# Optimization experiments

Measured on AMD Instinct MI355X. Metric: run time of the kernel, lower is better.

Reference implementation:

```python
import jax, jax.numpy as jnp
import numpy as np

D_MODEL = 1024
N_HEADS = 16
D_HEAD = 64


def setup_inputs() -> dict:
    key = jax.random.key(0)
    kx, kq, kk, kv, ko = jax.random.split(key, 5)
    B, T = 2, 2048
    inner = N_HEADS * D_HEAD
    s = 1.0 / np.sqrt(D_MODEL)
    return {
        "x": jax.random.normal(kx, (B, T, D_MODEL), dtype=jnp.float32),
        "Wq": jax.random.normal(kq, (D_MODEL, inner), dtype=jnp.float32) * s,
        "Wk": jax.random.normal(kk, (D_MODEL, inner), dtype=jnp.float32) * s,
        "Wv": jax.random.normal(kv, (D_MODEL, inner), dtype=jnp.float32) * s,
        "Wo": jax.random.normal(ko, (inner, D_MODEL), dtype=jnp.float32) * (1.0 / np.sqrt(inner)),
    }


def reference(x, Wq, Wk, Wv, Wo):
    B, T, D = x.shape
    H, d = N_HEADS, D_HEAD
    q = (x @ Wq).reshape(B, T, H, d)
    k = (x @ Wk).reshape(B, T, H, d)
    v = (x @ Wv).reshape(B, T, H, d)
    # scale=False -> no 1/sqrt(d) scaling
    scores = jnp.einsum('bthd,bshd->bhts', q, k)
    # strictly-lower-triangular mask (tril with diagonal=-1): s < t kept
    mask = jnp.tril(jnp.ones((T, T), dtype=bool), k=-1)
    scores = jnp.where(mask, scores, 0.0)
    out = jnp.einsum('bhts,bshd->bthd', scores, v).reshape(B, T, H * d)
    return out @ Wo
```

## Files before the change

kernel.cpp:

```cpp
#include <hip/hip_runtime.h>
#include <hip/hip_bf16.h>

#define TSEQ   2048
#define DM     1024
#define NHEAD  16
#define DH     64
#define BATCH  2
#define MR     (BATCH * TSEQ)
#define CH     64
#define NC     (TSEQ / CH)
#define QKVLD  (3 * DM)
#define LP     72

typedef __attribute__((ext_vector_type(8))) short bf16x8;
typedef __attribute__((ext_vector_type(4))) float f32x4;

__device__ __forceinline__ short f2bf(float x) {
  __hip_bfloat16 h = __float2bfloat16(x);
  return *reinterpret_cast<short*>(&h);
}

__device__ __forceinline__ void stage16(const void* g, void* l) {
  __builtin_amdgcn_global_load_lds(
      (const __attribute__((address_space(1))) void*)g,
      (__attribute__((address_space(3))) void*)l, 16, 0, 0);
}

__device__ __forceinline__ void store_elem(float v, float* p) { *p = v; }
__device__ __forceinline__ void store_elem(float v, __hip_bfloat16* p) { *p = __float2bfloat16(v); }

template <typename OutT>
__global__ __launch_bounds__(256) void gemm_bf16(const short* __restrict__ A,
                                                 const short* __restrict__ Bt,
                                                 OutT* __restrict__ C,
                                                 int M, int N, int K, int ldc) {
  __shared__ short As[128][32];
  __shared__ short Bs[128][32];
  const int tid = threadIdx.x;
  const int lane = tid & 63, wid = tid >> 6;
  const int wave_m = wid >> 1, wave_n = wid & 1;
  const int row0 = blockIdx.y * 128, col0 = blockIdx.x * 128;

  const int sr = tid >> 2, sk = (tid & 3) * 8;
  const short* Ag0 = A + (size_t)(row0 + sr) * K + sk;
  const short* Bg0 = Bt + (size_t)(col0 + sr) * K + sk;
  short* AsL = &As[0][0] + tid * 8;
  short* BsL = &Bs[0][0] + tid * 8;

  f32x4 acc[4][4];
#pragma unroll
  for (int i = 0; i < 4; ++i)
#pragma unroll
    for (int j = 0; j < 4; ++j) acc[i][j] = (f32x4){0.f, 0.f, 0.f, 0.f};

  const int fm = wave_m * 64 + (lane & 15);
  const int fn = wave_n * 64 + (lane & 15);
  const int fk = (lane >> 4) * 8;

  for (int k0 = 0; k0 < K; k0 += 32) {
    stage16(Ag0 + k0, AsL);
    stage16(Ag0 + (size_t)64 * K + k0, AsL + 2048);
    stage16(Bg0 + k0, BsL);
    stage16(Bg0 + (size_t)64 * K + k0, BsL + 2048);
    __syncthreads();
    bf16x8 af[4], bf[4];
#pragma unroll
    for (int t = 0; t < 4; ++t) {
      af[t] = *(const bf16x8*)&As[fm + t * 16][fk];
      bf[t] = *(const bf16x8*)&Bs[fn + t * 16][fk];
    }
#pragma unroll
    for (int im = 0; im < 4; ++im)
#pragma unroll
      for (int jn = 0; jn < 4; ++jn)
        acc[im][jn] = __builtin_amdgcn_mfma_f32_16x16x32_bf16(af[im], bf[jn], acc[im][jn], 0, 0, 0);
    __syncthreads();
  }

  const int crow = (lane >> 4) * 4, ccol = lane & 15;
#pragma unroll
  for (int im = 0; im < 4; ++im)
#pragma unroll
    for (int jn = 0; jn < 4; ++jn) {
      OutT* Cp = C + (size_t)(row0 + wave_m * 64 + im * 16 + crow) * ldc
                   + col0 + wave_n * 64 + jn * 16 + ccol;
#pragma unroll
      for (int r = 0; r < 4; ++r) store_elem(acc[im][jn][r], Cp + (size_t)r * ldc);
    }
}

__global__ __launch_bounds__(256) void cvt_bf16(const float* __restrict__ in,
                                                __hip_bfloat16* __restrict__ out, int n) {
  int i = (blockIdx.x * 256 + threadIdx.x) * 4;
  if (i >= n) return;
  float4 v = *(const float4*)(in + i);
  union { __hip_bfloat16 h[4]; uint2 u; } pk;
  pk.h[0] = __float2bfloat16(v.x); pk.h[1] = __float2bfloat16(v.y);
  pk.h[2] = __float2bfloat16(v.z); pk.h[3] = __float2bfloat16(v.w);
  *(uint2*)(out + i) = pk.u;
}

__global__ __launch_bounds__(256) void transposeW4(const float* __restrict__ W0,
                                                   const float* __restrict__ W1,
                                                   const float* __restrict__ W2,
                                                   const float* __restrict__ W3,
                                                   __hip_bfloat16* __restrict__ Wt) {
  const float* W = blockIdx.z == 0 ? W0 : blockIdx.z == 1 ? W1 : blockIdx.z == 2 ? W2 : W3;
  __hip_bfloat16* out = Wt + (size_t)blockIdx.z * DM * DM;
  __shared__ float tile[64][65];
  const int tid = threadIdx.x;
  const int kt = blockIdx.y * 64, nt = blockIdx.x * 64;
  const int lr = tid >> 6, lc = tid & 63;
#pragma unroll
  for (int i = 0; i < 16; ++i) {
    int k = i * 4 + lr;
    tile[k][lc] = W[(size_t)(kt + k) * DM + nt + lc];
  }
  __syncthreads();
  const int nl = tid >> 4, k4 = (tid & 15) * 4;
#pragma unroll
  for (int i = 0; i < 4; ++i) {
    int n = i * 16 + nl;
    union { __hip_bfloat16 h[4]; uint2 u; } pk;
#pragma unroll
    for (int x = 0; x < 4; ++x) pk.h[x] = __float2bfloat16(tile[k4 + x][n]);
    *(uint2*)(out + (size_t)(nt + n) * DM + kt + k4) = pk.u;
  }
}

__global__ __launch_bounds__(256) void chunk_kv(const __hip_bfloat16* __restrict__ QKV,
                                                float* __restrict__ Mc) {
  const int c = blockIdx.x, h = blockIdx.y, b = blockIdx.z;
  __shared__ short Kt[DH][LP];
  __shared__ short Vt[DH][LP];
  const int tid = threadIdx.x;
  const int lane = tid & 63, w = tid >> 6;
  const int r = tid >> 2, q16 = (tid & 3) * 16;
  const short* qkv = (const short*)QKV;
  const size_t grow = ((size_t)(b * TSEQ + c * CH + r)) * QKVLD + h * DH;
  short kk[16], vv[16];
  *(bf16x8*)&kk[0] = *(const bf16x8*)(qkv + grow + DM + q16);
  *(bf16x8*)&kk[8] = *(const bf16x8*)(qkv + grow + DM + q16 + 8);
  *(bf16x8*)&vv[0] = *(const bf16x8*)(qkv + grow + 2 * DM + q16);
  *(bf16x8*)&vv[8] = *(const bf16x8*)(qkv + grow + 2 * DM + q16 + 8);
#pragma unroll
  for (int j = 0; j < 16; ++j) {
    Kt[q16 + j][r] = kk[j];
    Vt[q16 + j][r] = vv[j];
  }
  __syncthreads();

  const int m = lane & 15, q = lane >> 4;
  bf16x8 af[2];
  af[0] = *(const bf16x8*)&Vt[16 * w + m][q * 8];
  af[1] = *(const bf16x8*)&Vt[16 * w + m][q * 8 + 32];
  f32x4 acc[4];
#pragma unroll
  for (int ct = 0; ct < 4; ++ct) acc[ct] = (f32x4){0.f, 0.f, 0.f, 0.f};
#pragma unroll
  for (int ct = 0; ct < 4; ++ct) {
    bf16x8 b0 = *(const bf16x8*)&Kt[ct * 16 + m][q * 8];
    bf16x8 b1 = *(const bf16x8*)&Kt[ct * 16 + m][q * 8 + 32];
    acc[ct] = __builtin_amdgcn_mfma_f32_16x16x32_bf16(af[0], b0, acc[ct], 0, 0, 0);
    acc[ct] = __builtin_amdgcn_mfma_f32_16x16x32_bf16(af[1], b1, acc[ct], 0, 0, 0);
  }
  float* out = Mc + ((size_t)((b * NHEAD + h) * NC + c)) * (DH * DH);
#pragma unroll
  for (int ct = 0; ct < 4; ++ct)
#pragma unroll
    for (int rr = 0; rr < 4; ++rr) {
      int row = 16 * w + q * 4 + rr, col = ct * 16 + m;
      out[(size_t)row * DH + col] = acc[ct][rr];
    }
}

__global__ __launch_bounds__(256) void scan_states(const float* __restrict__ Mc,
                                                   __hip_bfloat16* __restrict__ Spre) {
  const int bh = blockIdx.y;
  const size_t off = (size_t)bh * NC * (DH * DH) + blockIdx.x * 256 + threadIdx.x;
  const float* src = Mc + off;
  __hip_bfloat16* dst = Spre + off;
  float run = 0.f;
  for (int c = 0; c < NC; ++c) {
    dst[(size_t)c * (DH * DH)] = __float2bfloat16(run);
    run += src[(size_t)c * (DH * DH)];
  }
}

__global__ __launch_bounds__(256) void intra_attn(const __hip_bfloat16* __restrict__ QKV,
                                                  const __hip_bfloat16* __restrict__ Spre,
                                                  __hip_bfloat16* __restrict__ O_) {
  const int c = blockIdx.x, h = blockIdx.y, b = blockIdx.z;
  __shared__ short Qs[CH][LP];
  __shared__ short Ks[CH][LP];
  __shared__ short Vt[DH][LP];
  __shared__ short St[DH][LP];
  const int tid = threadIdx.x;
  const int lane = tid & 63, w = tid >> 6;
  const int r = tid >> 2, q16 = (tid & 3) * 16;
  const short* qkv = (const short*)QKV;
  const size_t grow = ((size_t)(b * TSEQ + c * CH + r)) * QKVLD + h * DH;
  *(bf16x8*)&Qs[r][q16]     = *(const bf16x8*)(qkv + grow + q16);
  *(bf16x8*)&Qs[r][q16 + 8] = *(const bf16x8*)(qkv + grow + q16 + 8);
  *(bf16x8*)&Ks[r][q16]     = *(const bf16x8*)(qkv + grow + DM + q16);
  *(bf16x8*)&Ks[r][q16 + 8] = *(const bf16x8*)(qkv + grow + DM + q16 + 8);
  const short* Sg = (const short*)Spre + ((size_t)((b * NHEAD + h) * NC + c)) * (DH * DH);
  *(bf16x8*)&St[r][q16]     = *(const bf16x8*)(Sg + r * DH + q16);
  *(bf16x8*)&St[r][q16 + 8] = *(const bf16x8*)(Sg + r * DH + q16 + 8);
  short vv[16];
  *(bf16x8*)&vv[0] = *(const bf16x8*)(qkv + grow + 2 * DM + q16);
  *(bf16x8*)&vv[8] = *(const bf16x8*)(qkv + grow + 2 * DM + q16 + 8);
#pragma unroll
  for (int j = 0; j < 16; ++j) Vt[q16 + j][r] = vv[j];
  __syncthreads();

  const int m = lane & 15, q = lane >> 4;
  bf16x8 af[2];
  af[0] = *(const bf16x8*)&Qs[16 * w + m][q * 8];
  af[1] = *(const bf16x8*)&Qs[16 * w + m][q * 8 + 32];
  f32x4 acc[4], pacc[4];
#pragma unroll
  for (int ct = 0; ct < 4; ++ct) {
    acc[ct] = (f32x4){0.f, 0.f, 0.f, 0.f};
    pacc[ct] = (f32x4){0.f, 0.f, 0.f, 0.f};
  }
#pragma unroll
  for (int ct = 0; ct < 4; ++ct) {
    bf16x8 s0 = *(const bf16x8*)&St[ct * 16 + m][q * 8];
    bf16x8 s1 = *(const bf16x8*)&St[ct * 16 + m][q * 8 + 32];
    acc[ct] = __builtin_amdgcn_mfma_f32_16x16x32_bf16(af[0], s0, acc[ct], 0, 0, 0);
    acc[ct] = __builtin_amdgcn_mfma_f32_16x16x32_bf16(af[1], s1, acc[ct], 0, 0, 0);
    bf16x8 k0 = *(const bf16x8*)&Ks[ct * 16 + m][q * 8];
    bf16x8 k1 = *(const bf16x8*)&Ks[ct * 16 + m][q * 8 + 32];
    pacc[ct] = __builtin_amdgcn_mfma_f32_16x16x32_bf16(af[0], k0, pacc[ct], 0, 0, 0);
    pacc[ct] = __builtin_amdgcn_mfma_f32_16x16x32_bf16(af[1], k1, pacc[ct], 0, 0, 0);
  }
  __syncthreads();
#pragma unroll
  for (int ct = 0; ct < 4; ++ct) {
    int col = ct * 16 + m;
#pragma unroll
    for (int rr = 0; rr < 4; ++rr) {
      int row = 16 * w + q * 4 + rr;
      float pv = (col < row) ? pacc[ct][rr] : 0.f;
      Qs[row][col] = f2bf(pv);
    }
  }
  __syncthreads();
  bf16x8 pf[2];
  pf[0] = *(const bf16x8*)&Qs[16 * w + m][q * 8];
  pf[1] = *(const bf16x8*)&Qs[16 * w + m][q * 8 + 32];
#pragma unroll
  for (int ct = 0; ct < 4; ++ct) {
    bf16x8 v0 = *(const bf16x8*)&Vt[ct * 16 + m][q * 8];
    bf16x8 v1 = *(const bf16x8*)&Vt[ct * 16 + m][q * 8 + 32];
    acc[ct] = __builtin_amdgcn_mfma_f32_16x16x32_bf16(pf[0], v0, acc[ct], 0, 0, 0);
    acc[ct] = __builtin_amdgcn_mfma_f32_16x16x32_bf16(pf[1], v1, acc[ct], 0, 0, 0);
  }
  __hip_bfloat16* Ob = O_ + ((size_t)(b * TSEQ + c * CH)) * DM + h * DH;
#pragma unroll
  for (int ct = 0; ct < 4; ++ct)
#pragma unroll
    for (int rr = 0; rr < 4; ++rr) {
      int row = 16 * w + q * 4 + rr, col = ct * 16 + m;
      Ob[(size_t)row * DM + col] = __float2bfloat16(acc[ct][rr]);
    }
}

extern "C" void kernel_launch(void* const* d_in, const int* in_sizes, int n_in,
                              void* d_out, int out_size, void* d_ws, size_t ws_size,
                              hipStream_t stream) {
  const float* x  = (const float*)d_in[0];
  const float* Wq = (const float*)d_in[1];
  const float* Wk = (const float*)d_in[2];
  const float* Wv = (const float*)d_in[3];
  const float* Wo = (const float*)d_in[4];
  float* out = (float*)d_out;

  char* ws = (char*)d_ws;
  __hip_bfloat16* xb    = (__hip_bfloat16*)ws;  ws += (size_t)MR * DM * 2;
  __hip_bfloat16* WtAll = (__hip_bfloat16*)ws;  ws += (size_t)4 * DM * DM * 2;
  __hip_bfloat16* qkvb  = (__hip_bfloat16*)ws;  ws += (size_t)MR * QKVLD * 2;
  float*          Mc    = (float*)ws;           ws += (size_t)BATCH * NHEAD * NC * DH * DH * 4;
  __hip_bfloat16* Spre  = (__hip_bfloat16*)ws;  ws += (size_t)BATCH * NHEAD * NC * DH * DH * 2;
  __hip_bfloat16* aob   = (__hip_bfloat16*)ws;  ws += (size_t)MR * DM * 2;

  cvt_bf16<<<(MR * DM / 4 + 255) / 256, 256, 0, stream>>>(x, xb, MR * DM);
  transposeW4<<<dim3(DM / 64, DM / 64, 4), 256, 0, stream>>>(Wq, Wk, Wv, Wo, WtAll);

  gemm_bf16<__hip_bfloat16><<<dim3(QKVLD / 128, MR / 128), 256, 0, stream>>>(
      (const short*)xb, (const short*)WtAll, qkvb, MR, QKVLD, DM, QKVLD);

  chunk_kv<<<dim3(NC, NHEAD, BATCH), 256, 0, stream>>>(qkvb, Mc);
  scan_states<<<dim3(DH * DH / 256, BATCH * NHEAD), 256, 0, stream>>>(Mc, Spre);
  intra_attn<<<dim3(NC, NHEAD, BATCH), 256, 0, stream>>>(qkvb, Spre, aob);

  gemm_bf16<float><<<dim3(DM / 128, MR / 128), 256, 0, stream>>>(
      (const short*)aob, (const short*)(WtAll + (size_t)3 * DM * DM), out, MR, DM, DM, DM);
}
```

Baseline: 170.2 us.

## Emit chunk-transposed K/V from QKV GEMM and merge prep kernels

The QKV GEMM epilogue now writes Q and K row-major and also writes K and V in per-(batch, head, chunk) transposed 64x64 tiles. chunk_kv and intra_attn can then read MFMA fragments straight from global memory, with no LDS transposes and fewer barriers. intra_attn is reordered to compute transposed outputs so it can use packed stores. The x conversion and weight transposes are merged into one prep launch. The cost is extra global writes of K, plus more workspace and 8-byte strided scattered stores in the GEMM epilogue.

```diff
diff --git a/kernel.cpp b/kernel.cpp
--- a/kernel.cpp
+++ b/kernel.cpp
@@ -26,14 +26,13 @@
       (__attribute__((address_space(3))) void*)l, 16, 0, 0);
 }
 
-__device__ __forceinline__ void store_elem(float v, float* p) { *p = v; }
-__device__ __forceinline__ void store_elem(float v, __hip_bfloat16* p) { *p = __float2bfloat16(v); }
-
-template <typename OutT>
-__global__ __launch_bounds__(256) void gemm_bf16(const short* __restrict__ A,
-                                                 const short* __restrict__ Bt,
-                                                 OutT* __restrict__ C,
-                                                 int M, int N, int K, int ldc) {
+__global__ __launch_bounds__(256) void gemm_qkv(const short* __restrict__ A,
+                                                const short* __restrict__ Bt,
+                                                short* __restrict__ qb,
+                                                short* __restrict__ kb,
+                                                short* __restrict__ kT,
+                                                short* __restrict__ vT) {
+  const int K = DM;
   __shared__ short As[128][32];
   __shared__ short Bs[128][32];
   const int tid = threadIdx.x;
@@ -78,37 +77,127 @@
   }
 
   const int crow = (lane >> 4) * 4, ccol = lane & 15;
+  const int region = col0 >> 10;
+
+  if (region <= 1) {
+    short* Cb = (region == 0) ? qb : kb;
+#pragma unroll
+    for (int im = 0; im < 4; ++im)
+#pragma unroll
+      for (int jn = 0; jn < 4; ++jn) {
+        const int gr = row0 + wave_m * 64 + im * 16 + crow;
+        const int gc = (col0 & 1023) + wave_n * 64 + jn * 16 + ccol;
+        short* Cp = Cb + (size_t)gr * DM + gc;
+#pragma unroll
+        for (int r = 0; r < 4; ++r) Cp[(size_t)r * DM] = f2bf(acc[im][jn][r]);
+      }
+  }
+  if (region >= 1) {
+    short* Tt = (region == 1) ? kT : vT;
+    const int gr0 = row0 + wave_m * 64;
+    const int b = gr0 >> 11;
+    const int c = (gr0 & 2047) >> 6;
+#pragma unroll
+    for (int im = 0; im < 4; ++im)
+#pragma unroll
+      for (int jn = 0; jn < 4; ++jn) {
+        const int gcol = (col0 & 1023) + wave_n * 64 + jn * 16 + ccol;
+        const int h = gcol >> 6, i = gcol & 63;
+        const int s0 = im * 16 + crow;
+        size_t idx = ((((size_t)(b * NHEAD + h) * NC + c) * DH + i) * DH + s0);
+        union { short h4[4]; uint2 u; } pk;
+#pragma unroll
+        for (int r = 0; r < 4; ++r) pk.h4[r] = f2bf(acc[im][jn][r]);
+        *(uint2*)(Tt + idx) = pk.u;
+      }
+  }
+}
+
+__global__ __launch_bounds__(256) void gemm_out(const short* __restrict__ A,
+                                                const short* __restrict__ Bt,
+                                                float* __restrict__ C) {
+  const int K = DM, N = DM;
+  __shared__ short As[128][32];
+  __shared__ short Bs[128][32];
+  const int tid = threadIdx.x;
+  const int lane = tid & 63, wid = tid >> 6;
+  const int wave_m = wid >> 1, wave_n = wid & 1;
+  const int row0 = blockIdx.y * 128, col0 = blockIdx.x * 128;
+
+  const int sr = tid >> 2, sk = (tid & 3) * 8;
+  const short* Ag0 = A + (size_t)(row0 + sr) * K + sk;
+  const short* Bg0 = Bt + (size_t)(col0 + sr) * K + sk;
+  short* AsL = &As[0][0] + tid * 8;
+  short* BsL = &Bs[0][0] + tid * 8;
+
+  f32x4 acc[4][4];
+#pragma unroll
+  for (int i = 0; i < 4; ++i)
+#pragma unroll
+    for (int j = 0; j < 4; ++j) acc[i][j] = (f32x4){0.f, 0.f, 0.f, 0.f};
+
+  const int fm = wave_m * 64 + (lane & 15);
+  const int fn = wave_n * 64 + (lane & 15);
+  const int fk = (lane >> 4) * 8;
+
+  for (int k0 = 0; k0 < K; k0 += 32) {
+    stage16(Ag0 + k0, AsL);
+    stage16(Ag0 + (size_t)64 * K + k0, AsL + 2048);
+    stage16(Bg0 + k0, BsL);
+    stage16(Bg0 + (size_t)64 * K + k0, BsL + 2048);
+    __syncthreads();
+    bf16x8 af[4], bf[4];
+#pragma unroll
+    for (int t = 0; t < 4; ++t) {
+      af[t] = *(const bf16x8*)&As[fm + t * 16][fk];
+      bf[t] = *(const bf16x8*)&Bs[fn + t * 16][fk];
+    }
+#pragma unroll
+    for (int im = 0; im < 4; ++im)
+#pragma unroll
+      for (int jn = 0; jn < 4; ++jn)
+        acc[im][jn] = __builtin_amdgcn_mfma_f32_16x16x32_bf16(af[im], bf[jn], acc[im][jn], 0, 0, 0);
+    __syncthreads();
+  }
+
+  const int crow = (lane >> 4) * 4, ccol = lane & 15;
 #pragma unroll
   for (int im = 0; im < 4; ++im)
 #pragma unroll
     for (int jn = 0; jn < 4; ++jn) {
-      OutT* Cp = C + (size_t)(row0 + wave_m * 64 + im * 16 + crow) * ldc
-                   + col0 + wave_n * 64 + jn * 16 + ccol;
-#pragma unroll
-      for (int r = 0; r < 4; ++r) store_elem(acc[im][jn][r], Cp + (size_t)r * ldc);
-    }
-}
-
-__global__ __launch_bounds__(256) void cvt_bf16(const float* __restrict__ in,
-                                                __hip_bfloat16* __restrict__ out, int n) {
-  int i = (blockIdx.x * 256 + threadIdx.x) * 4;
-  if (i >= n) return;
-  float4 v = *(const float4*)(in + i);
-  union { __hip_bfloat16 h[4]; uint2 u; } pk;
-  pk.h[0] = __float2bfloat16(v.x); pk.h[1] = __float2bfloat16(v.y);
-  pk.h[2] = __float2bfloat16(v.z); pk.h[3] = __float2bfloat16(v.w);
-  *(uint2*)(out + i) = pk.u;
-}
-
-__global__ __launch_bounds__(256) void transposeW4(const float* __restrict__ W0,
-                                                   const float* __restrict__ W1,
-                                                   const float* __restrict__ W2,
-                                                   const float* __restrict__ W3,
-                                                   __hip_bfloat16* __restrict__ Wt) {
+      float* Cp = C + (size_t)(row0 + wave_m * 64 + im * 16 + crow) * N
+                    + col0 + wave_n * 64 + jn * 16 + ccol;
+#pragma unroll
+      for (int r = 0; r < 4; ++r) Cp[(size_t)r * N] = acc[im][jn][r];
+    }
+}
+
+__global__ __launch_bounds__(256) void prep(const float* __restrict__ x,
+                                            const float* __restrict__ W0,
+                                            const float* __restrict__ W1,
+                                            const float* __restrict__ W2,
+                                            const float* __restrict__ W3,
+                                            __hip_bfloat16* __restrict__ xb,
+                                            __hip_bfloat16* __restrict__ Wt) {
+  const int tid = threadIdx.x;
+  if (blockIdx.z == 4) {
+    const int bid = blockIdx.y * 16 + blockIdx.x;
+    const float* src = x + (size_t)bid * 16384;
+    __hip_bfloat16* dst = xb + (size_t)bid * 16384;
+#pragma unroll
+    for (int it = 0; it < 16; ++it) {
+      int i = it * 1024 + tid * 4;
+      float4 v = *(const float4*)(src + i);
+      union { __hip_bfloat16 h[4]; uint2 u; } pk;
+      pk.h[0] = __float2bfloat16(v.x); pk.h[1] = __float2bfloat16(v.y);
+      pk.h[2] = __float2bfloat16(v.z); pk.h[3] = __float2bfloat16(v.w);
+      *(uint2*)(dst + i) = pk.u;
+    }
+    return;
+  }
   const float* W = blockIdx.z == 0 ? W0 : blockIdx.z == 1 ? W1 : blockIdx.z == 2 ? W2 : W3;
   __hip_bfloat16* out = Wt + (size_t)blockIdx.z * DM * DM;
   __shared__ float tile[64][65];
-  const int tid = threadIdx.x;
   const int kt = blockIdx.y * 64, nt = blockIdx.x * 64;
   const int lr = tid >> 6, lc = tid & 63;
 #pragma unroll
@@ -123,55 +212,38 @@
     int n = i * 16 + nl;
     union { __hip_bfloat16 h[4]; uint2 u; } pk;
 #pragma unroll
-    for (int x = 0; x < 4; ++x) pk.h[x] = __float2bfloat16(tile[k4 + x][n]);
+    for (int xx = 0; xx < 4; ++xx) pk.h[xx] = __float2bfloat16(tile[k4 + xx][n]);
     *(uint2*)(out + (size_t)(nt + n) * DM + kt + k4) = pk.u;
   }
 }
 
-__global__ __launch_bounds__(256) void chunk_kv(const __hip_bfloat16* __restrict__ QKV,
+__global__ __launch_bounds__(256) void chunk_kv(const short* __restrict__ kT,
+                                                const short* __restrict__ vT,
                                                 float* __restrict__ Mc) {
   const int c = blockIdx.x, h = blockIdx.y, b = blockIdx.z;
-  __shared__ short Kt[DH][LP];
-  __shared__ short Vt[DH][LP];
-  const int tid = threadIdx.x;
-  const int lane = tid & 63, w = tid >> 6;
-  const int r = tid >> 2, q16 = (tid & 3) * 16;
-  const short* qkv = (const short*)QKV;
-  const size_t grow = ((size_t)(b * TSEQ + c * CH + r)) * QKVLD + h * DH;
-  short kk[16], vv[16];
-  *(bf16x8*)&kk[0] = *(const bf16x8*)(qkv + grow + DM + q16);
-  *(bf16x8*)&kk[8] = *(const bf16x8*)(qkv + grow + DM + q16 + 8);
-  *(bf16x8*)&vv[0] = *(const bf16x8*)(qkv + grow + 2 * DM + q16);
-  *(bf16x8*)&vv[8] = *(const bf16x8*)(qkv + grow + 2 * DM + q16 + 8);
-#pragma unroll
-  for (int j = 0; j < 16; ++j) {
-    Kt[q16 + j][r] = kk[j];
-    Vt[q16 + j][r] = vv[j];
-  }
-  __syncthreads();
-
+  const size_t tile = ((size_t)(b * NHEAD + h) * NC + c) * (DH * DH);
+  const int tid = threadIdx.x, lane = tid & 63, w = tid >> 6;
   const int m = lane & 15, q = lane >> 4;
-  bf16x8 af[2];
-  af[0] = *(const bf16x8*)&Vt[16 * w + m][q * 8];
-  af[1] = *(const bf16x8*)&Vt[16 * w + m][q * 8 + 32];
+  const short* vt = vT + tile;
+  const short* kt = kT + tile;
+  bf16x8 a0 = *(const bf16x8*)(vt + (16 * w + m) * DH + q * 8);
+  bf16x8 a1 = *(const bf16x8*)(vt + (16 * w + m) * DH + q * 8 + 32);
   f32x4 acc[4];
 #pragma unroll
   for (int ct = 0; ct < 4; ++ct) acc[ct] = (f32x4){0.f, 0.f, 0.f, 0.f};
 #pragma unroll
   for (int ct = 0; ct < 4; ++ct) {
-    bf16x8 b0 = *(const bf16x8*)&Kt[ct * 16 + m][q * 8];
-    bf16x8 b1 = *(const bf16x8*)&Kt[ct * 16 + m][q * 8 + 32];
-    acc[ct] = __builtin_amdgcn_mfma_f32_16x16x32_bf16(af[0], b0, acc[ct], 0, 0, 0);
-    acc[ct] = __builtin_amdgcn_mfma_f32_16x16x32_bf16(af[1], b1, acc[ct], 0, 0, 0);
-  }
-  float* out = Mc + ((size_t)((b * NHEAD + h) * NC + c)) * (DH * DH);
+    bf16x8 b0 = *(const bf16x8*)(kt + (ct * 16 + m) * DH + q * 8);
+    bf16x8 b1 = *(const bf16x8*)(kt + (ct * 16 + m) * DH + q * 8 + 32);
+    acc[ct] = __builtin_amdgcn_mfma_f32_16x16x32_bf16(a0, b0, acc[ct], 0, 0, 0);
+    acc[ct] = __builtin_amdgcn_mfma_f32_16x16x32_bf16(a1, b1, acc[ct], 0, 0, 0);
+  }
+  float* out = Mc + tile;
 #pragma unroll
   for (int ct = 0; ct < 4; ++ct)
 #pragma unroll
-    for (int rr = 0; rr < 4; ++rr) {
-      int row = 16 * w + q * 4 + rr, col = ct * 16 + m;
-      out[(size_t)row * DH + col] = acc[ct][rr];
-    }
+    for (int rr = 0; rr < 4; ++rr)
+      out[(size_t)(16 * w + q * 4 + rr) * DH + ct * 16 + m] = acc[ct][rr];
 }
 
 __global__ __launch_bounds__(256) void scan_states(const float* __restrict__ Mc,
@@ -187,37 +259,34 @@
   }
 }
 
-__global__ __launch_bounds__(256) void intra_attn(const __hip_bfloat16* __restrict__ QKV,
-                                                  const __hip_bfloat16* __restrict__ Spre,
-                                                  __hip_bfloat16* __restrict__ O_) {
+__global__ __launch_bounds__(256) void intra_attn(const short* __restrict__ qb,
+                                                  const short* __restrict__ kb,
+                                                  const short* __restrict__ vT,
+                                                  const short* __restrict__ Spre,
+                                                  short* __restrict__ O_) {
   const int c = blockIdx.x, h = blockIdx.y, b = blockIdx.z;
   __shared__ short Qs[CH][LP];
   __shared__ short Ks[CH][LP];
-  __shared__ short Vt[DH][LP];
-  __shared__ short St[DH][LP];
-  const int tid = threadIdx.x;
-  const int lane = tid & 63, w = tid >> 6;
+  const int tid = threadIdx.x, lane = tid & 63, w = tid >> 6;
+  const int m = lane & 15, q = lane >> 4;
   const int r = tid >> 2, q16 = (tid & 3) * 16;
-  const short* qkv = (const short*)QKV;
-  const size_t grow = ((size_t)(b * TSEQ + c * CH + r)) * QKVLD + h * DH;
-  *(bf16x8*)&Qs[r][q16]     = *(const bf16x8*)(qkv + grow + q16);
-  *(bf16x8*)&Qs[r][q16 + 8] = *(const bf16x8*)(qkv + grow + q16 + 8);
-  *(bf16x8*)&Ks[r][q16]     = *(const bf16x8*)(qkv + grow + DM + q16);
-  *(bf16x8*)&Ks[r][q16 + 8] = *(const bf16x8*)(qkv + grow + DM + q16 + 8);
-  const short* Sg = (const short*)Spre + ((size_t)((b * NHEAD + h) * NC + c)) * (DH * DH);
-  *(bf16x8*)&St[r][q16]     = *(const bf16x8*)(Sg + r * DH + q16);
-  *(bf16x8*)&St[r][q16 + 8] = *(const bf16x8*)(Sg + r * DH + q16 + 8);
-  short vv[16];
-  *(bf16x8*)&vv[0] = *(const bf16x8*)(qkv + grow + 2 * DM + q16);
-  *(bf16x8*)&vv[8] = *(const bf16x8*)(qkv + grow + 2 * DM + q16 + 8);
-#pragma unroll
-  for (int j = 0; j < 16; ++j) Vt[q16 + j][r] = vv[j];
+  const size_t tile = ((size_t)(b * NHEAD + h) * NC + c) * (DH * DH);
+  const size_t grow = ((size_t)(b * TSEQ + c * CH + r)) * DM + h * DH;
+  *(bf16x8*)&Qs[r][q16]     = *(const bf16x8*)(qb + grow + q16);
+  *(bf16x8*)&Qs[r][q16 + 8] = *(const bf16x8*)(qb + grow + q16 + 8);
+  *(bf16x8*)&Ks[r][q16]     = *(const bf16x8*)(kb + grow + q16);
+  *(bf16x8*)&Ks[r][q16 + 8] = *(const bf16x8*)(kb + grow + q16 + 8);
+  const short* vt = vT + tile;
+  const short* st = Spre + tile;
+  bf16x8 av0 = *(const bf16x8*)(vt + (16 * w + m) * DH + q * 8);
+  bf16x8 av1 = *(const bf16x8*)(vt + (16 * w + m) * DH + q * 8 + 32);
+  bf16x8 as0 = *(const bf16x8*)(st + (16 * w + m) * DH + q * 8);
+  bf16x8 as1 = *(const bf16x8*)(st + (16 * w + m) * DH + q * 8 + 32);
   __syncthreads();
 
-  const int m = lane & 15, q = lane >> 4;
-  bf16x8 af[2];
-  af[0] = *(const bf16x8*)&Qs[16 * w + m][q * 8];
-  af[1] = *(const bf16x8*)&Qs[16 * w + m][q * 8 + 32];
+  bf16x8 aq0 = *(const bf16x8*)&Qs[16 * w + m][q * 8];
+  bf16x8 aq1 = *(const bf16x8*)&Qs[16 * w + m][q * 8 + 32];
+
   f32x4 acc[4], pacc[4];
 #pragma unroll
   for (int ct = 0; ct < 4; ++ct) {
@@ -226,45 +295,41 @@
   }
 #pragma unroll
   for (int ct = 0; ct < 4; ++ct) {
-    bf16x8 s0 = *(const bf16x8*)&St[ct * 16 + m][q * 8];
-    bf16x8 s1 = *(const bf16x8*)&St[ct * 16 + m][q * 8 + 32];
-    acc[ct] = __builtin_amdgcn_mfma_f32_16x16x32_bf16(af[0], s0, acc[ct], 0, 0, 0);
-    acc[ct] = __builtin_amdgcn_mfma_f32_16x16x32_bf16(af[1], s1, acc[ct], 0, 0, 0);
-    bf16x8 k0 = *(const bf16x8*)&Ks[ct * 16 + m][q * 8];
-    bf16x8 k1 = *(const bf16x8*)&Ks[ct * 16 + m][q * 8 + 32];
-    pacc[ct] = __builtin_amdgcn_mfma_f32_16x16x32_bf16(af[0], k0, pacc[ct], 0, 0, 0);
-    pacc[ct] = __builtin_amdgcn_mfma_f32_16x16x32_bf16(af[1], k1, pacc[ct], 0, 0, 0);
+    bf16x8 bq0 = *(const bf16x8*)&Qs[ct * 16 + m][q * 8];
+    bf16x8 bq1 = *(const bf16x8*)&Qs[ct * 16 + m][q * 8 + 32];
+    acc[ct] = __builtin_amdgcn_mfma_f32_16x16x32_bf16(as0, bq0, acc[ct], 0, 0, 0);
+    acc[ct] = __builtin_amdgcn_mfma_f32_16x16x32_bf16(as1, bq1, acc[ct], 0, 0, 0);
+    bf16x8 bk0 = *(const bf16x8*)&Ks[ct * 16 + m][q * 8];
+    bf16x8 bk1 = *(const bf16x8*)&Ks[ct * 16 + m][q * 8 + 32];
+    pacc[ct] = __builtin_amdgcn_mfma_f32_16x16x32_bf16(aq0, bk0, pacc[ct], 0, 0, 0);
+    pacc[ct] = __builtin_amdgcn_mfma_f32_16x16x32_bf16(aq1, bk1, pacc[ct], 0, 0, 0);
   }
   __syncthreads();
 #pragma unroll
   for (int ct = 0; ct < 4; ++ct) {
-    int col = ct * 16 + m;
+    const int s = ct * 16 + m;
 #pragma unroll
     for (int rr = 0; rr < 4; ++rr) {
-      int row = 16 * w + q * 4 + rr;
-      float pv = (col < row) ? pacc[ct][rr] : 0.f;
-      Qs[row][col] = f2bf(pv);
+      const int t = 16 * w + q * 4 + rr;
+      Ks[t][s] = f2bf((s < t) ? pacc[ct][rr] : 0.f);
     }
   }
   __syncthreads();
-  bf16x8 pf[2];
-  pf[0] = *(const bf16x8*)&Qs[16 * w + m][q * 8];
-  pf[1] = *(const bf16x8*)&Qs[16 * w + m][q * 8 + 32];
-#pragma unroll
-  for (int ct = 0; ct < 4; ++ct) {
-    bf16x8 v0 = *(const bf16x8*)&Vt[ct * 16 + m][q * 8];
-    bf16x8 v1 = *(const bf16x8*)&Vt[ct * 16 + m][q * 8 + 32];
-    acc[ct] = __builtin_amdgcn_mfma_f32_16x16x32_bf16(pf[0], v0, acc[ct], 0, 0, 0);
-    acc[ct] = __builtin_amdgcn_mfma_f32_16x16x32_bf16(pf[1], v1, acc[ct], 0, 0, 0);
-  }
-  __hip_bfloat16* Ob = O_ + ((size_t)(b * TSEQ + c * CH)) * DM + h * DH;
-#pragma unroll
-  for (int ct = 0; ct < 4; ++ct)
-#pragma unroll
-    for (int rr = 0; rr < 4; ++rr) {
-      int row = 16 * w + q * 4 + rr, col = ct * 16 + m;
-      Ob[(size_t)row * DM + col] = __float2bfloat16(acc[ct][rr]);
-    }
+#pragma unroll
+  for (int ct = 0; ct < 4; ++ct) {
+    bf16x8 bp0 = *(const bf16x8*)&Ks[ct * 16 + m][q * 8];
+    bf16x8 bp1 = *(const bf16x8*)&Ks[ct * 16 + m][q * 8 + 32];
+    acc[ct] = __builtin_amdgcn_mfma_f32_16x16x32_bf16(av0, bp0, acc[ct], 0, 0, 0);
+    acc[ct] = __builtin_amdgcn_mfma_f32_16x16x32_bf16(av1, bp1, acc[ct], 0, 0, 0);
+  }
+#pragma unroll
+  for (int ct = 0; ct < 4; ++ct) {
+    const int t = ct * 16 + m, j0 = 16 * w + q * 4;
+    union { short h4[4]; uint2 u; } pk;
+#pragma unroll
+    for (int rr = 0; rr < 4; ++rr) pk.h4[rr] = f2bf(acc[ct][rr]);
+    *(uint2*)(O_ + ((size_t)(b * TSEQ + c * CH + t)) * DM + h * DH + j0) = pk.u;
+  }
 }
 
 extern "C" void kernel_launch(void* const* d_in, const int* in_sizes, int n_in,
@@ -278,23 +343,26 @@
   float* out = (float*)d_out;
 
   char* ws = (char*)d_ws;
-  __hip_bfloat16* xb    = (__hip_bfloat16*)ws;  ws += (size_t)MR * DM * 2;
-  __hip_bfloat16* WtAll = (__hip_bfloat16*)ws;  ws += (size_t)4 * DM * DM * 2;
-  __hip_bfloat16* qkvb  = (__hip_bfloat16*)ws;  ws += (size_t)MR * QKVLD * 2;
-  float*          Mc    = (float*)ws;           ws += (size_t)BATCH * NHEAD * NC * DH * DH * 4;
-  __hip_bfloat16* Spre  = (__hip_bfloat16*)ws;  ws += (size_t)BATCH * NHEAD * NC * DH * DH * 2;
-  __hip_bfloat16* aob   = (__hip_bfloat16*)ws;  ws += (size_t)MR * DM * 2;
-
-  cvt_bf16<<<(MR * DM / 4 + 255) / 256, 256, 0, stream>>>(x, xb, MR * DM);
-  transposeW4<<<dim3(DM / 64, DM / 64, 4), 256, 0, stream>>>(Wq, Wk, Wv, Wo, WtAll);
-
-  gemm_bf16<__hip_bfloat16><<<dim3(QKVLD / 128, MR / 128), 256, 0, stream>>>(
-      (const short*)xb, (const short*)WtAll, qkvb, MR, QKVLD, DM, QKVLD);
-
-  chunk_kv<<<dim3(NC, NHEAD, BATCH), 256, 0, stream>>>(qkvb, Mc);
-  scan_states<<<dim3(DH * DH / 256, BATCH * NHEAD), 256, 0, stream>>>(Mc, Spre);
-  intra_attn<<<dim3(NC, NHEAD, BATCH), 256, 0, stream>>>(qkvb, Spre, aob);
-
-  gemm_bf16<float><<<dim3(DM / 128, MR / 128), 256, 0, stream>>>(
-      (const short*)aob, (const short*)(WtAll + (size_t)3 * DM * DM), out, MR, DM, DM, DM);
-}
+  short* xb    = (short*)ws;  ws += (size_t)MR * DM * 2;
+  short* WtAll = (short*)ws;  ws += (size_t)4 * DM * DM * 2;
+  short* qb    = (short*)ws;  ws += (size_t)MR * DM * 2;
+  short* kb    = (short*)ws;  ws += (size_t)MR * DM * 2;
+  short* kT    = (short*)ws;  ws += (size_t)MR * DM * 2;
+  short* vT    = (short*)ws;  ws += (size_t)MR * DM * 2;
+  float* Mc    = (float*)ws;  ws += (size_t)MR * DM * 4;
+  short* Spre  = (short*)ws;  ws += (size_t)MR * DM * 2;
+  short* aob   = (short*)ws;  ws += (size_t)MR * DM * 2;
+
+  prep<<<dim3(16, 16, 5), 256, 0, stream>>>(x, Wq, Wk, Wv, Wo,
+                                            (__hip_bfloat16*)xb, (__hip_bfloat16*)WtAll);
+
+  gemm_qkv<<<dim3(QKVLD / 128, MR / 128), 256, 0, stream>>>(xb, WtAll, qb, kb, kT, vT);
+
+  chunk_kv<<<dim3(NC, NHEAD, BATCH), 256, 0, stream>>>(kT, vT, Mc);
+  scan_states<<<dim3(DH * DH / 256, BATCH * NHEAD), 256, 0, stream>>>(
+      Mc, (__hip_bfloat16*)Spre);
+  intra_attn<<<dim3(NC, NHEAD, BATCH), 256, 0, stream>>>(qb, kb, vT, Spre, aob);
+
+  gemm_out<<<dim3(DM / 128, MR / 128), 256, 0, stream>>>(
+      aob, WtAll + (size_t)3 * DM * DM, out);
+}
```

After: 170.8 us. Within noise of the previous version (+0.3%).
